# Kernel tuning notes

Hardware: AMD Instinct MI355X
Metric: run time of the kernel (lower is better)

Reference implementation:

```python
import jax, jax.numpy as jnp
import numpy as np

# dims: N nodes, E edges, C channel multiplicity, NS species, RB radial basis, H radial mlp hidden
N, E, C, NS, RB, H = 4000, 128000, 128, 5, 8, 64
AVG_N = 32.0  # avg_n_neighbors


def setup_inputs() -> dict:
    key = jax.random.key(0)
    ks = jax.random.split(key, 17)
    return {
        "x_scalars": jax.random.normal(ks[0], (N, C), jnp.float32),
        "x_vectors": jax.random.normal(ks[1], (N, C, 3), jnp.float32),
        "edge_vectors": jax.random.normal(ks[2], (E, 3), jnp.float32) * 2.0,
        "radial_basis": jax.random.normal(ks[3], (E, RB), jnp.float32),
        "W1_0": jax.random.normal(ks[4], (C, C), jnp.float32),
        "W1_1": jax.random.normal(ks[5], (C, C), jnp.float32),
        "rmlp_w0": jax.random.normal(ks[6], (RB, H), jnp.float32) * np.float32(np.sqrt(4.0 / RB)),
        "rmlp_w1": jax.random.normal(ks[7], (H, H), jnp.float32) * np.float32(np.sqrt(4.0 / H)),
        "rmlp_w2": jax.random.normal(ks[8], (H, H), jnp.float32) * np.float32(np.sqrt(4.0 / H)),
        "rmlp_w3": jax.random.normal(ks[9], (H, 4 * C), jnp.float32) * np.float32(np.sqrt(1.0 / H)),
        "W2_0": jax.random.normal(ks[10], (2 * C, 2 * C), jnp.float32),
        "W2_1": jax.random.normal(ks[11], (2 * C, C), jnp.float32),
        "Wsk0": jax.random.normal(ks[12], (NS, C, 2 * C), jnp.float32),
        "Wsk1": jax.random.normal(ks[13], (NS, C, C), jnp.float32),
        "species": jax.random.randint(ks[14], (N,), 0, NS),
        "senders": jax.random.randint(ks[15], (E,), 0, N),
        "receivers": jax.random.randint(ks[16], (E,), 0, N),
    }


def reference(x_scalars, x_vectors, edge_vectors, radial_basis,
              W1_0, W1_1, rmlp_w0, rmlp_w1, rmlp_w2, rmlp_w3,
              W2_0, W2_1, Wsk0, Wsk1, species, senders, receivers):
    n_nodes = x_scalars.shape[0]
    inv_c = 1.0 / jnp.sqrt(jnp.float32(C))
    # linear_1: per-irrep channel mixing (e3nn path-normalized Linear)
    y0 = (x_scalars @ W1_0) * inv_c                                  # [N,C] 0e
    y1 = jnp.einsum('nci,cd->ndi', x_vectors, W1_1) * inv_c          # [N,C,3] 1o
    # gather to edges
    m0 = y0[senders]                                                 # [E,C]
    m1 = y1[senders]                                                 # [E,C,3]
    # spherical harmonics lmax=1, component normalization: Y0=1, Y1=sqrt(3)*unit_vec
    r = jnp.linalg.norm(edge_vectors, axis=1, keepdims=True)
    u = edge_vectors / jnp.maximum(r, 1e-12)
    Y1 = jnp.sqrt(3.0) * u                                           # [E,3]
    # tensor product filtered to 0e,1o (explicit Clebsch-Gordan, component norm)
    t0a = m0                                                         # 0e x 0e -> 0e
    t0b = jnp.einsum('eci,ei->ec', m1, Y1) / jnp.sqrt(3.0)           # 1o x 1o -> 0e
    t1a = m0[:, :, None] * Y1[:, None, :]                            # 0e x 1o -> 1o
    t1b = m1                                                         # 1o x 0e -> 1o
    # radial MLP (silu, no bias), one scalar weight per tp irrep (4C total)
    h = jax.nn.silu(radial_basis @ rmlp_w0)
    h = jax.nn.silu(h @ rmlp_w1)
    h = jax.nn.silu(h @ rmlp_w2)
    w = h @ rmlp_w3                                                  # [E,4C]
    ws0, ws1 = w[:, :C], w[:, C:2 * C]
    wv0, wv1 = w[:, 2 * C:3 * C], w[:, 3 * C:]
    scal = jnp.concatenate([t0a * ws0, t0b * ws1], axis=1)           # [E,2C]
    vec = jnp.concatenate([t1a * wv0[:, :, None], t1b * wv1[:, :, None]], axis=1)  # [E,2C,3]
    # scatter-add to receivers, neighbor normalization
    inv_nb = 1.0 / jnp.sqrt(jnp.float32(AVG_N))
    agg_s = jax.ops.segment_sum(scal, receivers, num_segments=n_nodes) * inv_nb
    agg_v = jax.ops.segment_sum(vec, receivers, num_segments=n_nodes) * inv_nb
    # linear_2: tp irreps -> (2C)x0e + Cx1o  (C output scalars + C gates)
    inv_2c = 1.0 / jnp.sqrt(jnp.float32(2 * C))
    s = (agg_s @ W2_0) * inv_2c                                      # [N,2C]
    v = jnp.einsum('nci,cd->ndi', agg_v, W2_1) * inv_2c              # [N,C,3]
    # indexed (per-species) skip connection
    s = s + jnp.einsum('nc,ncd->nd', x_scalars, Wsk0[species]) * inv_c
    v = v + jnp.einsum('nci,ncd->ndi', x_vectors, Wsk1[species]) * inv_c
    # gate: silu on scalars, silu(gates) multiplies 1o features
    out_s = jax.nn.silu(s[:, :C])
    gates = jax.nn.silu(s[:, C:])
    out_v = v * gates[:, :, None]
    return jnp.concatenate([out_s, out_v.reshape(n_nodes, 3 * C)], axis=1)  # [N,4C]
```

## Files before the change

### kernel.cpp

```cpp
#include <hip/hip_runtime.h>
#include <math.h>

#define CC 128
#define HH 64
#define RBD 8
#define WDIM 512

typedef __attribute__((ext_vector_type(8))) short short8v;
typedef __attribute__((ext_vector_type(4))) float f32x4;

__device__ __forceinline__ float silu_f(float x) {
    return x / (1.0f + __expf(-x));
}

__device__ __forceinline__ unsigned short f2bf(float x) {
    unsigned int b = __float_as_uint(x);
    unsigned int r = (b + 0x7FFFu + ((b >> 16) & 1u)) >> 16;
    return (unsigned short)r;
}

__device__ __forceinline__ float bf2f(unsigned short u) {
    return __uint_as_float(((unsigned int)u) << 16);
}

__global__ void k_prep_hist(const float* __restrict__ w0, const float* __restrict__ w1,
                            const float* __restrict__ w2, const float* __restrict__ w3,
                            float* __restrict__ w0T, float* __restrict__ w1T,
                            float* __restrict__ w2T, float* __restrict__ w3T,
                            unsigned short* __restrict__ w3bs,
                            unsigned short* __restrict__ w0b,
                            unsigned short* __restrict__ w1b,
                            unsigned short* __restrict__ w2b,
                            const int* __restrict__ rcv, int* __restrict__ deg, int E_,
                            const int* __restrict__ species, int* __restrict__ scnt, int N) {
    int i = blockIdx.x * blockDim.x + threadIdx.x;
    if (i < E_) atomicAdd(&deg[rcv[i]], 1);
    if (i < N) atomicAdd(&scnt[species[i]], 1);
    if (i < 64 * 8) { int m = i / 8, k = i % 8; w0T[i] = w0[k * 64 + m]; }
    if (i < 64 * 64) { int m = i / 64, k = i % 64; w1T[i] = w1[k * 64 + m]; w2T[i] = w2[k * 64 + m]; }
    if (i < 512 * 64) { int j = i / 64, k = i % 64; w3T[i] = w3[k * 512 + j]; }
    if (i < 32768) {
        int t = i >> 10, ch = (i >> 9) & 1, lane = (i >> 3) & 63, j = i & 7;
        int k = ch * 32 + 8 * (lane >> 4) + j;
        int n = t * 16 + (lane & 15);
        w3bs[i] = f2bf(w3[k * 512 + n]);
    }
    if (i < 2048) {
        int t = i >> 9, lane = (i >> 3) & 63, j = i & 7;
        int k = 8 * (lane >> 4) + j;
        int col = t * 16 + (lane & 15);
        w0b[i] = (k < RBD) ? f2bf(w0[k * 64 + col]) : (unsigned short)0;
    }
    if (i < 4096) {
        int f = i >> 9, lane = (i >> 3) & 63, j = i & 7;
        int ks = f >> 2, t = f & 3;
        int k = ks * 32 + 8 * (lane >> 4) + j;
        int col = t * 16 + (lane & 15);
        w1b[i] = f2bf(w1[k * 64 + col]);
        w2b[i] = f2bf(w2[k * 64 + col]);
    }
}

__global__ __launch_bounds__(1024) void k_scan(const int* __restrict__ deg,
                                               int* __restrict__ off, int N,
                                               const int* __restrict__ scnt,
                                               int* __restrict__ soff, int NS) {
    __shared__ int s[1024];
    int t = threadIdx.x;
    int b = t * 4;
    int a0 = (b + 0 < N) ? deg[b + 0] : 0;
    int a1 = (b + 1 < N) ? deg[b + 1] : 0;
    int a2 = (b + 2 < N) ? deg[b + 2] : 0;
    int a3 = (b + 3 < N) ? deg[b + 3] : 0;
    int part = a0 + a1 + a2 + a3;
    s[t] = part;
    __syncthreads();
    for (int d = 1; d < 1024; d <<= 1) {
        int v = (t >= d) ? s[t - d] : 0;
        __syncthreads();
        s[t] += v;
        __syncthreads();
    }
    int excl = s[t] - part;
    if (b + 0 <= N) off[b + 0] = excl;
    if (b + 1 <= N) off[b + 1] = excl + a0;
    if (b + 2 <= N) off[b + 2] = excl + a0 + a1;
    if (b + 3 <= N) off[b + 3] = excl + a0 + a1 + a2;
    if (t == 0) {
        int acc = 0;
        for (int q = 0; q < NS; q++) { soff[q] = acc; acc += scnt[q]; }
        soff[NS] = acc;
    }
}

__global__ void k_scatter(const int* __restrict__ rcv, const int* __restrict__ off,
                          int* __restrict__ cur, int* __restrict__ elist, int E_,
                          const int* __restrict__ species, const int* __restrict__ soff,
                          int* __restrict__ scur, int* __restrict__ nlist, int N) {
    int e = blockIdx.x * blockDim.x + threadIdx.x;
    if (e < E_) {
        int r = rcv[e];
        int p = atomicAdd(&cur[r], 1);
        elist[off[r] + p] = e;
    }
    if (e < N) {
        int s = species[e];
        int p = atomicAdd(&scur[s], 1);
        nlist[soff[s] + p] = e;
    }
}

__global__ __launch_bounds__(256) void k_node_lin(
    const float* __restrict__ xs, const float* __restrict__ xv,
    const float* __restrict__ W10, const float* __restrict__ W11,
    float* __restrict__ y0, float* __restrict__ y1, int N) {
    const int tid = threadIdx.x;
    const int n0 = blockIdx.x * 2;
    const int NP = N * CC;
    const int d = tid & 127;
    const int nn = tid >> 7;
    const float inv_c = 0.08838834764831845f;

    __shared__ float xsl[2][128];
    __shared__ float xvl[2][384];
    xsl[tid >> 7][tid & 127] = xs[(size_t)n0 * 128 + tid];
    for (int i = tid; i < 768; i += 256) xvl[i / 384][i % 384] = xv[(size_t)n0 * 384 + i];
    __syncthreads();

    float a0 = 0.f, av0 = 0.f, av1 = 0.f, av2 = 0.f;
    #pragma unroll 4
    for (int c = 0; c < CC; c++) {
        float w10 = W10[c * CC + d];
        float w11 = W11[c * CC + d];
        float xsv = xsl[nn][c];
        a0 += xsv * w10;
        av0 += xvl[nn][c * 3 + 0] * w11;
        av1 += xvl[nn][c * 3 + 1] * w11;
        av2 += xvl[nn][c * 3 + 2] * w11;
    }
    y0[(size_t)(n0 + nn) * CC + d] = a0 * inv_c;
    y1[0 * NP + (size_t)(n0 + nn) * CC + d] = av0 * inv_c;
    y1[1 * NP + (size_t)(n0 + nn) * CC + d] = av1 * inv_c;
    y1[2 * NP + (size_t)(n0 + nn) * CC + d] = av2 * inv_c;
}

__device__ __forceinline__ void layer64(const float4* a, float4* b,
                                        const float* __restrict__ W) {
    #pragma unroll
    for (int m = 0; m < 16; m++) {
        float s0 = 0.f, s1 = 0.f, s2 = 0.f, s3 = 0.f;
        const float* w0p = W + (4 * m + 0) * 64;
        const float* w1p = W + (4 * m + 1) * 64;
        const float* w2p = W + (4 * m + 2) * 64;
        const float* w3p = W + (4 * m + 3) * 64;
        #pragma unroll
        for (int k = 0; k < 16; k++) {
            float4 av = a[k];
            s0 += av.x * w0p[4 * k + 0] + av.y * w0p[4 * k + 1] + av.z * w0p[4 * k + 2] + av.w * w0p[4 * k + 3];
            s1 += av.x * w1p[4 * k + 0] + av.y * w1p[4 * k + 1] + av.z * w1p[4 * k + 2] + av.w * w1p[4 * k + 3];
            s2 += av.x * w2p[4 * k + 0] + av.y * w2p[4 * k + 1] + av.z * w2p[4 * k + 2] + av.w * w2p[4 * k + 3];
            s3 += av.x * w3p[4 * k + 0] + av.y * w3p[4 * k + 1] + av.z * w3p[4 * k + 2] + av.w * w3p[4 * k + 3];
        }
        b[m] = make_float4(silu_f(s0), silu_f(s1), silu_f(s2), silu_f(s3));
    }
}

__device__ __forceinline__ void mlp_body(
    const float* __restrict__ rb, int e,
    const float* __restrict__ w0T, const float* __restrict__ w1T,
    const float* __restrict__ w2T, float4* a) {
    float rbv[RBD];
    #pragma unroll
    for (int k = 0; k < RBD; k++) rbv[k] = rb[(size_t)e * RBD + k];
    float4 b[16];
    #pragma unroll
    for (int m = 0; m < 16; m++) {
        float s0 = 0.f, s1 = 0.f, s2 = 0.f, s3 = 0.f;
        #pragma unroll
        for (int k = 0; k < RBD; k++) {
            float rv = rbv[k];
            s0 += rv * w0T[(4 * m + 0) * RBD + k];
            s1 += rv * w0T[(4 * m + 1) * RBD + k];
            s2 += rv * w0T[(4 * m + 2) * RBD + k];
            s3 += rv * w0T[(4 * m + 3) * RBD + k];
        }
        a[m] = make_float4(silu_f(s0), silu_f(s1), silu_f(s2), silu_f(s3));
    }
    layer64(a, b, w1T);
    layer64(b, a, w2T);
}

__global__ __launch_bounds__(256) void k_mlpw3(
    const float* __restrict__ rb, const int* __restrict__ elist,
    const int* __restrict__ snd, const float* __restrict__ evec,
    const unsigned short* __restrict__ w0b, const unsigned short* __restrict__ w1b,
    const unsigned short* __restrict__ w2b, const unsigned short* __restrict__ w3bs,
    unsigned int* __restrict__ Wq, float4* __restrict__ up, int* __restrict__ sp,
    int E_, int nblk_mlp,
    const float* __restrict__ xs, const float* __restrict__ xv,
    const float* __restrict__ W10, const float* __restrict__ W11,
    float* __restrict__ y0, float* __restrict__ y1, int NP) {
    __shared__ unsigned short hbuf[4][16][72];
    __shared__ float xsl[2][128];
    __shared__ float xvl[2][384];

    if (blockIdx.x >= nblk_mlp) {
        const int tid = threadIdx.x;
        const int n0 = (blockIdx.x - nblk_mlp) * 2;
        const int d = tid & 127;
        const int nn = tid >> 7;
        const float inv_c = 0.08838834764831845f;

        xsl[tid >> 7][tid & 127] = xs[(size_t)n0 * 128 + tid];
        for (int i = tid; i < 768; i += 256) xvl[i / 384][i % 384] = xv[(size_t)n0 * 384 + i];
        __syncthreads();

        float a0 = 0.f, av0 = 0.f, av1 = 0.f, av2 = 0.f;
        #pragma unroll 4
        for (int c = 0; c < CC; c++) {
            float w10 = W10[c * CC + d];
            float w11 = W11[c * CC + d];
            float xsv = xsl[nn][c];
            a0 += xsv * w10;
            av0 += xvl[nn][c * 3 + 0] * w11;
            av1 += xvl[nn][c * 3 + 1] * w11;
            av2 += xvl[nn][c * 3 + 2] * w11;
        }
        y0[(size_t)(n0 + nn) * CC + d] = a0 * inv_c;
        y1[0 * NP + (size_t)(n0 + nn) * CC + d] = av0 * inv_c;
        y1[1 * NP + (size_t)(n0 + nn) * CC + d] = av1 * inv_c;
        y1[2 * NP + (size_t)(n0 + nn) * CC + d] = av2 * inv_c;
        return;
    }

    const int lane = threadIdx.x & 63;
    const int wv = threadIdx.x >> 6;
    const int rbk = blockIdx.x * 4 + wv;
    const int col = lane & 15;
    const int grp = lane >> 4;

    if (threadIdx.x < 64) {
        int p = blockIdx.x * 64 + threadIdx.x;
        if (p < E_) {
            int e = elist[p];
            float e0 = evec[(size_t)e * 3 + 0];
            float e1 = evec[(size_t)e * 3 + 1];
            float e2 = evec[(size_t)e * 3 + 2];
            float rn = sqrtf(e0 * e0 + e1 * e1 + e2 * e2);
            float inv = 1.0f / fmaxf(rn, 1e-12f);
            up[p] = make_float4(e0 * inv, e1 * inv, e2 * inv, 0.f);
            sp[p] = snd[e];
        }
    }

    short8v a0 = (short8v){0, 0, 0, 0, 0, 0, 0, 0};
    if (grp == 0) {
        int e = elist[rbk * 16 + col];
        const float* rp = rb + (size_t)e * RBD;
        #pragma unroll
        for (int j = 0; j < RBD; j++) a0[j] = (short)f2bf(rp[j]);
    }
    f32x4 acc[4];
    {
        const unsigned short* bp = w0b + (size_t)lane * 8;
        #pragma unroll
        for (int t = 0; t < 4; t++) {
            short8v b = *(const short8v*)(bp + (size_t)t * 512);
            acc[t] = __builtin_amdgcn_mfma_f32_16x16x32_bf16(
                a0, b, (f32x4){0.f, 0.f, 0.f, 0.f}, 0, 0, 0);
        }
    }
    #pragma unroll
    for (int t = 0; t < 4; t++)
        #pragma unroll
        for (int r = 0; r < 4; r++)
            hbuf[wv][grp * 4 + r][t * 16 + col] = f2bf(silu_f(acc[t][r]));

    {
        short8v aA = *(const short8v*)&hbuf[wv][col][8 * grp];
        short8v aB = *(const short8v*)&hbuf[wv][col][32 + 8 * grp];
        const unsigned short* bp = w1b + (size_t)lane * 8;
        #pragma unroll
        for (int t = 0; t < 4; t++) {
            short8v b0 = *(const short8v*)(bp + (size_t)(0 + t) * 512);
            short8v b1 = *(const short8v*)(bp + (size_t)(4 + t) * 512);
            f32x4 c = __builtin_amdgcn_mfma_f32_16x16x32_bf16(
                aA, b0, (f32x4){0.f, 0.f, 0.f, 0.f}, 0, 0, 0);
            acc[t] = __builtin_amdgcn_mfma_f32_16x16x32_bf16(aB, b1, c, 0, 0, 0);
        }
    }
    #pragma unroll
    for (int t = 0; t < 4; t++)
        #pragma unroll
        for (int r = 0; r < 4; r++)
            hbuf[wv][grp * 4 + r][t * 16 + col] = f2bf(silu_f(acc[t][r]));

    {
        short8v aA = *(const short8v*)&hbuf[wv][col][8 * grp];
        short8v aB = *(const short8v*)&hbuf[wv][col][32 + 8 * grp];
        const unsigned short* bp = w2b + (size_t)lane * 8;
        #pragma unroll
        for (int t = 0; t < 4; t++) {
            short8v b0 = *(const short8v*)(bp + (size_t)(0 + t) * 512);
            short8v b1 = *(const short8v*)(bp + (size_t)(4 + t) * 512);
            f32x4 c = __builtin_amdgcn_mfma_f32_16x16x32_bf16(
                aA, b0, (f32x4){0.f, 0.f, 0.f, 0.f}, 0, 0, 0);
            acc[t] = __builtin_amdgcn_mfma_f32_16x16x32_bf16(aB, b1, c, 0, 0, 0);
        }
    }
    #pragma unroll
    for (int t = 0; t < 4; t++)
        #pragma unroll
        for (int r = 0; r < 4; r++)
            hbuf[wv][grp * 4 + r][t * 16 + col] = f2bf(silu_f(acc[t][r]));

    short8v A0 = *(const short8v*)&hbuf[wv][col][8 * grp];
    short8v A1 = *(const short8v*)&hbuf[wv][col][32 + 8 * grp];

    const unsigned short* bbase = w3bs + (size_t)lane * 8;
    const int rowq = grp * 4;
    const int jbase = rbk * 16 + rowq;

    #pragma unroll 1
    for (int pass = 0; pass < 2; pass++) {
        f32x4 wacc[16];
        #pragma unroll
        for (int q = 0; q < 16; q++) wacc[q] = (f32x4){0.f, 0.f, 0.f, 0.f};
        #pragma unroll
        for (int q = 0; q < 16; q++) {
            int t = (q < 8) ? (pass * 8 + q) : (16 + pass * 8 + (q - 8));
            short8v b0 = *(const short8v*)(bbase + (size_t)(t * 2 + 0) * 512);
            short8v b1 = *(const short8v*)(bbase + (size_t)(t * 2 + 1) * 512);
            wacc[q] = __builtin_amdgcn_mfma_f32_16x16x32_bf16(A0, b0, wacc[q], 0, 0, 0);
            wacc[q] = __builtin_amdgcn_mfma_f32_16x16x32_bf16(A1, b1, wacc[q], 0, 0, 0);
        }
        #pragma unroll
        for (int q = 0; q < 8; q++) {
            int t = pass * 8 + q;
            #pragma unroll
            for (int rr = 0; rr < 4; rr++) {
                unsigned lo = f2bf(wacc[q][rr]);
                unsigned hi = f2bf(wacc[q + 8][rr]);
                Wq[(size_t)(jbase + rr) * 256 + t * 16 + col] = lo | (hi << 16);
            }
        }
    }
}

__global__ __launch_bounds__(256, 4) void k_gather_em(
    const int* __restrict__ off, const float4* __restrict__ up,
    const int* __restrict__ sp, const unsigned int* __restrict__ Wq,
    const float* __restrict__ y0, const float* __restrict__ y1, int NP,
    float* __restrict__ agg_s, float* __restrict__ agg_v) {
    const int r = blockIdx.x;
    const int tid = threadIdx.x;
    const int half = tid >> 7;
    const int c = tid & 127;
    const int start = off[r];
    const int end = off[r + 1];

    float accs = 0.f, av0 = 0.f, av1 = 0.f, av2 = 0.f;
    const float SQ3 = 1.7320508075688772f;

    auto proc = [&](unsigned wq, float4 u, int s) {
        float wa = bf2f((unsigned short)(wq & 0xFFFFu));
        float wb = bf2f((unsigned short)(wq >> 16));
        if (half == 0) {
            float f = y0[(size_t)s * CC + c];
            accs += f * wa;
            float bb = f * wb * SQ3;
            av0 += bb * u.x; av1 += bb * u.y; av2 += bb * u.z;
        } else {
            float f0 = y1[0 * NP + s * CC + c];
            float f1 = y1[1 * NP + s * CC + c];
            float f2 = y1[2 * NP + s * CC + c];
            accs += (f0 * u.x + f1 * u.y + f2 * u.z) * wa;
            av0 += f0 * wb; av1 += f1 * wb; av2 += f2 * wb;
        }
    };

    int j = start;
    for (; j + 4 <= end; j += 4) {
        unsigned wq0 = Wq[(size_t)(j + 0) * 256 + tid];
        unsigned wq1 = Wq[(size_t)(j + 1) * 256 + tid];
        unsigned wq2 = Wq[(size_t)(j + 2) * 256 + tid];
        unsigned wq3 = Wq[(size_t)(j + 3) * 256 + tid];
        float4 u0 = up[j + 0], u1 = up[j + 1], u2 = up[j + 2], u3 = up[j + 3];
        int s0 = __builtin_amdgcn_readfirstlane(sp[j + 0]);
        int s1 = __builtin_amdgcn_readfirstlane(sp[j + 1]);
        int s2 = __builtin_amdgcn_readfirstlane(sp[j + 2]);
        int s3 = __builtin_amdgcn_readfirstlane(sp[j + 3]);
        proc(wq0, u0, s0);
        proc(wq1, u1, s1);
        proc(wq2, u2, s2);
        proc(wq3, u3, s3);
    }
    for (; j < end; j++) {
        unsigned wq = Wq[(size_t)j * 256 + tid];
        float4 u = up[j];
        int s = __builtin_amdgcn_readfirstlane(sp[j]);
        proc(wq, u, s);
    }

    agg_s[(size_t)r * 256 + tid] = accs;
    float* o = agg_v + ((size_t)r * 256 + tid) * 3;
    o[0] = av0; o[1] = av1; o[2] = av2;
}

__global__ __launch_bounds__(256) void k_mlp_wp(
    const float* __restrict__ rb, const int* __restrict__ elist,
    const float* __restrict__ w0T, const float* __restrict__ w1T,
    const float* __restrict__ w2T, const float* __restrict__ w3T,
    unsigned short* __restrict__ Wp, int E_) {
    int p = blockIdx.x * blockDim.x + threadIdx.x;
    if (p >= E_) return;
    int e = elist[p];
    const int c0 = blockIdx.y * 128;

    float4 a[16];
    mlp_body(rb, e, w0T, w1T, w2T, a);

    const size_t E4 = (size_t)E_ * 4;
    for (int c = c0; c < c0 + 128; c += 8) {
        float s[8];
        #pragma unroll
        for (int q = 0; q < 8; q++) {
            const float* rp = w3T + (size_t)(c + q) * 64;
            float t0 = 0.f, t1 = 0.f, t2 = 0.f, t3 = 0.f;
            #pragma unroll
            for (int k = 0; k < 16; k++) {
                float4 h = a[k];
                t0 += h.x * rp[4 * k + 0];
                t1 += h.y * rp[4 * k + 1];
                t2 += h.z * rp[4 * k + 2];
                t3 += h.w * rp[4 * k + 3];
            }
            s[q] = (t0 + t1) + (t2 + t3);
        }
        ushort4 pk0 = make_ushort4(f2bf(s[0]), f2bf(s[1]), f2bf(s[2]), f2bf(s[3]));
        ushort4 pk1 = make_ushort4(f2bf(s[4]), f2bf(s[5]), f2bf(s[6]), f2bf(s[7]));
        *(ushort4*)(Wp + (size_t)(c >> 2) * E4 + (size_t)p * 4) = pk0;
        *(ushort4*)(Wp + (size_t)((c >> 2) + 1) * E4 + (size_t)p * 4) = pk1;
    }
}

__global__ __launch_bounds__(512, 2) void k_gather_wg(
    const int* __restrict__ off, const int* __restrict__ elist,
    const int* __restrict__ snd, const float* __restrict__ evec,
    const unsigned short* __restrict__ Wp, int E_,
    const float* __restrict__ y0, const float* __restrict__ y1, int NP,
    float* __restrict__ agg_s, float* __restrict__ agg_v) {
    const int r = blockIdx.x;
    const int tid = threadIdx.x;
    const int part = tid >> 7;
    const int c = tid & 127;

    const int start = off[r];
    const int end = off[r + 1];

    const unsigned short* __restrict__ wstream =
        Wp + (size_t)(tid >> 2) * ((size_t)E_ * 4) + (tid & 3);

    float acc0 = 0.f, acc1 = 0.f, acc2 = 0.f;
    const float SQ3 = 1.7320508075688772f;

    #pragma unroll 2
    for (int j = start; j < end; j++) {
        int e = elist[j];
        e = __builtin_amdgcn_readfirstlane(e);
        int s = snd[e];
        s = __builtin_amdgcn_readfirstlane(s);

        float e0 = evec[(size_t)e * 3 + 0];
        float e1 = evec[(size_t)e * 3 + 1];
        float e2 = evec[(size_t)e * 3 + 2];
        float rn = sqrtf(e0 * e0 + e1 * e1 + e2 * e2);
        float inv = 1.0f / fmaxf(rn, 1e-12f);
        float ux = e0 * inv, uy = e1 * inv, uz = e2 * inv;

        float w = bf2f(wstream[(size_t)j * 4]);

        if (part == 0) {
            acc0 += y0[(size_t)s * CC + c] * w;
        } else if (part == 1) {
            float f = y1[0 * NP + s * CC + c] * ux
                    + y1[1 * NP + s * CC + c] * uy
                    + y1[2 * NP + s * CC + c] * uz;
            acc0 += f * w;
        } else if (part == 2) {
            float bb = y0[(size_t)s * CC + c] * w * SQ3;
            acc0 += bb * ux; acc1 += bb * uy; acc2 += bb * uz;
        } else {
            acc0 += y1[0 * NP + s * CC + c] * w;
            acc1 += y1[1 * NP + s * CC + c] * w;
            acc2 += y1[2 * NP + s * CC + c] * w;
        }
    }

    if (part == 0) {
        agg_s[(size_t)r * 256 + c] = acc0;
    } else if (part == 1) {
        agg_s[(size_t)r * 256 + 128 + c] = acc0;
    } else if (part == 2) {
        float* o = agg_v + ((size_t)r * 256 + c) * 3;
        o[0] = acc0; o[1] = acc1; o[2] = acc2;
    } else {
        float* o = agg_v + ((size_t)r * 256 + 128 + c) * 3;
        o[0] = acc0; o[1] = acc1; o[2] = acc2;
    }
}

__global__ void k_mlp(const float* __restrict__ rb,
                      const float* __restrict__ w0T, const float* __restrict__ w1T,
                      const float* __restrict__ w2T,
                      float* __restrict__ h2, int E_) {
    int e = blockIdx.x * blockDim.x + threadIdx.x;
    if (e >= E_) return;
    float4 a[16];
    mlp_body(rb, e, w0T, w1T, w2T, a);
    float4* out = (float4*)(h2 + (size_t)e * HH);
    #pragma unroll
    for (int q = 0; q < 16; q++) out[q] = a[q];
}

__global__ __launch_bounds__(512, 1) void k_gather_h2(
    const int* __restrict__ off, const int* __restrict__ elist,
    const int* __restrict__ snd, const float* __restrict__ evec,
    const float* __restrict__ h2, const float* __restrict__ w3T,
    const float* __restrict__ y0, const float* __restrict__ y1, int NP,
    float* __restrict__ agg_s, float* __restrict__ agg_v) {
    const int r = blockIdx.x;
    const int tid = threadIdx.x;
    const int part = tid >> 7;
    const int c = tid & 127;

    const float4* wp = (const float4*)(w3T + (size_t)tid * 64);
    const int start = off[r];
    const int end = off[r + 1];

    float acc0 = 0.f, acc1 = 0.f, acc2 = 0.f;
    const float SQ3 = 1.7320508075688772f;

    for (int j = start; j < end; j++) {
        int e = elist[j];
        e = __builtin_amdgcn_readfirstlane(e);
        int s = snd[e];
        s = __builtin_amdgcn_readfirstlane(s);

        float e0 = evec[(size_t)e * 3 + 0];
        float e1 = evec[(size_t)e * 3 + 1];
        float e2 = evec[(size_t)e * 3 + 2];
        float rn = sqrtf(e0 * e0 + e1 * e1 + e2 * e2);
        float inv = 1.0f / fmaxf(rn, 1e-12f);
        float ux = e0 * inv, uy = e1 * inv, uz = e2 * inv;

        const float4* __restrict__ hp = (const float4*)(h2 + ((size_t)e << 6));
        float ws0 = 0.f, ws1 = 0.f, ws2 = 0.f, ws3 = 0.f;
        #pragma unroll
        for (int k = 0; k < 16; k++) {
            float4 h = hp[k];
            float4 wv = wp[k];
            ws0 += h.x * wv.x; ws1 += h.y * wv.y; ws2 += h.z * wv.z; ws3 += h.w * wv.w;
        }
        float w = (ws0 + ws1) + (ws2 + ws3);

        if (part == 0) {
            acc0 += y0[(size_t)s * CC + c] * w;
        } else if (part == 1) {
            float f = y1[0 * NP + s * CC + c] * ux
                    + y1[1 * NP + s * CC + c] * uy
                    + y1[2 * NP + s * CC + c] * uz;
            acc0 += f * w;
        } else if (part == 2) {
            float bb = y0[(size_t)s * CC + c] * w * SQ3;
            acc0 += bb * ux; acc1 += bb * uy; acc2 += bb * uz;
        } else {
            acc0 += y1[0 * NP + s * CC + c] * w;
            acc1 += y1[1 * NP + s * CC + c] * w;
            acc2 += y1[2 * NP + s * CC + c] * w;
        }
    }

    if (part == 0) {
        agg_s[(size_t)r * 256 + c] = acc0;
    } else if (part == 1) {
        agg_s[(size_t)r * 256 + 128 + c] = acc0;
    } else if (part == 2) {
        float* o = agg_v + ((size_t)r * 256 + c) * 3;
        o[0] = acc0; o[1] = acc1; o[2] = acc2;
    } else {
        float* o = agg_v + ((size_t)r * 256 + 128 + c) * 3;
        o[0] = acc0; o[1] = acc1; o[2] = acc2;
    }
}

__global__ __launch_bounds__(256) void k_node_out(
    const float* __restrict__ agg_s, const float* __restrict__ agg_v,
    const float* __restrict__ xs, const float* __restrict__ xv,
    const float* __restrict__ W20, const float* __restrict__ W21,
    const float* __restrict__ Wsk0, const float* __restrict__ Wsk1,
    const int* __restrict__ nlist, const int* __restrict__ species,
    float* __restrict__ out, int N) {
    const int tid = threadIdx.x;
    const int b0 = blockIdx.x * 4;
    const int nid0 = nlist[min(b0 + 0, N - 1)];
    const int nid1 = nlist[min(b0 + 1, N - 1)];
    const int nid2 = nlist[min(b0 + 2, N - 1)];
    const int nid3 = nlist[min(b0 + 3, N - 1)];

    __shared__ float as_l[4 * 256];
    __shared__ float av_l[4 * 768];
    __shared__ float xs_l[4 * 128];
    __shared__ float xv_l[4 * 384];
    __shared__ float s_l[4 * 256];

    {
        as_l[0 * 256 + tid] = agg_s[(size_t)nid0 * 256 + tid];
        as_l[1 * 256 + tid] = agg_s[(size_t)nid1 * 256 + tid];
        as_l[2 * 256 + tid] = agg_s[(size_t)nid2 * 256 + tid];
        as_l[3 * 256 + tid] = agg_s[(size_t)nid3 * 256 + tid];
        for (int i = tid; i < 768; i += 256) {
            av_l[0 * 768 + i] = agg_v[(size_t)nid0 * 768 + i];
            av_l[1 * 768 + i] = agg_v[(size_t)nid1 * 768 + i];
            av_l[2 * 768 + i] = agg_v[(size_t)nid2 * 768 + i];
            av_l[3 * 768 + i] = agg_v[(size_t)nid3 * 768 + i];
        }
        if (tid < 128) {
            xs_l[0 * 128 + tid] = xs[(size_t)nid0 * 128 + tid];
            xs_l[1 * 128 + tid] = xs[(size_t)nid1 * 128 + tid];
            xs_l[2 * 128 + tid] = xs[(size_t)nid2 * 128 + tid];
            xs_l[3 * 128 + tid] = xs[(size_t)nid3 * 128 + tid];
        }
        for (int i = tid; i < 384; i += 256) {
            xv_l[0 * 384 + i] = xv[(size_t)nid0 * 384 + i];
            xv_l[1 * 384 + i] = xv[(size_t)nid1 * 384 + i];
            xv_l[2 * 384 + i] = xv[(size_t)nid2 * 384 + i];
            xv_l[3 * 384 + i] = xv[(size_t)nid3 * 384 + i];
        }
    }
    const int sp0 = species[nid0], sp1 = species[nid1];
    const int sp2 = species[nid2], sp3 = species[nid3];
    const bool uni = (sp0 == sp1) && (sp1 == sp2) && (sp2 == sp3);
    __syncthreads();

    const float k_mat = 0.17677669529663687f * 0.0625f;
    const float inv_c = 0.08838834764831845f;

    {
        const int d = tid;
        float am[4] = {0.f, 0.f, 0.f, 0.f};
        for (int cc = 0; cc < 256; cc++) {
            float w = W20[cc * 256 + d];
            #pragma unroll
            for (int n = 0; n < 4; n++) am[n] += as_l[n * 256 + cc] * w;
        }
        float ak[4] = {0.f, 0.f, 0.f, 0.f};
        if (uni) {
            for (int cc = 0; cc < 128; cc++) {
                float w = Wsk0[((size_t)sp0 * 128 + cc) * 256 + d];
                #pragma unroll
                for (int n = 0; n < 4; n++) ak[n] += xs_l[n * 128 + cc] * w;
            }
        } else {
            for (int cc = 0; cc < 128; cc++) {
                float w0v = Wsk0[((size_t)sp0 * 128 + cc) * 256 + d];
                float w1v = Wsk0[((size_t)sp1 * 128 + cc) * 256 + d];
                float w2v = Wsk0[((size_t)sp2 * 128 + cc) * 256 + d];
                float w3v = Wsk0[((size_t)sp3 * 128 + cc) * 256 + d];
                ak[0] += xs_l[0 * 128 + cc] * w0v;
                ak[1] += xs_l[1 * 128 + cc] * w1v;
                ak[2] += xs_l[2 * 128 + cc] * w2v;
                ak[3] += xs_l[3 * 128 + cc] * w3v;
            }
        }
        #pragma unroll
        for (int n = 0; n < 4; n++) s_l[n * 256 + d] = am[n] * k_mat + ak[n] * inv_c;
    }
    __syncthreads();

    if (tid < 128) {
        out[(size_t)nid0 * 512 + tid] = silu_f(s_l[0 * 256 + tid]);
        out[(size_t)nid1 * 512 + tid] = silu_f(s_l[1 * 256 + tid]);
        out[(size_t)nid2 * 512 + tid] = silu_f(s_l[2 * 256 + tid]);
        out[(size_t)nid3 * 512 + tid] = silu_f(s_l[3 * 256 + tid]);
    }

    {
        const int d = tid & 127;
        const int half = tid >> 7;
        const int nA = half ? nid2 : nid0;
        const int nB = half ? nid3 : nid1;
        const int sA = half ? sp2 : sp0;
        const int sB = half ? sp3 : sp1;
        const int la = half ? 2 : 0;
        const int lb = half ? 3 : 1;

        float am[2][3] = {};
        for (int cc = 0; cc < 256; cc++) {
            float w = W21[cc * 128 + d];
            #pragma unroll
            for (int i = 0; i < 3; i++) {
                am[0][i] += av_l[la * 768 + cc * 3 + i] * w;
                am[1][i] += av_l[lb * 768 + cc * 3 + i] * w;
            }
        }
        float ak[2][3] = {};
        if (uni) {
            for (int cc = 0; cc < 128; cc++) {
                float w = Wsk1[((size_t)sp0 * 128 + cc) * 128 + d];
                #pragma unroll
                for (int i = 0; i < 3; i++) {
                    ak[0][i] += xv_l[la * 384 + cc * 3 + i] * w;
                    ak[1][i] += xv_l[lb * 384 + cc * 3 + i] * w;
                }
            }
        } else {
            for (int cc = 0; cc < 128; cc++) {
                float wA = Wsk1[((size_t)sA * 128 + cc) * 128 + d];
                float wB = Wsk1[((size_t)sB * 128 + cc) * 128 + d];
                #pragma unroll
                for (int i = 0; i < 3; i++) {
                    ak[0][i] += xv_l[la * 384 + cc * 3 + i] * wA;
                    ak[1][i] += xv_l[lb * 384 + cc * 3 + i] * wB;
                }
            }
        }
        float gA = silu_f(s_l[la * 256 + 128 + d]);
        float gB = silu_f(s_l[lb * 256 + 128 + d]);
        float* oA = out + (size_t)nA * 512 + 128 + d * 3;
        float* oB = out + (size_t)nB * 512 + 128 + d * 3;
        #pragma unroll
        for (int i = 0; i < 3; i++) {
            oA[i] = (am[0][i] * k_mat + ak[0][i] * inv_c) * gA;
            oB[i] = (am[1][i] * k_mat + ak[1][i] * inv_c) * gB;
        }
    }
}

extern "C" void kernel_launch(void* const* d_in, const int* in_sizes, int n_in,
                              void* d_out, int out_size, void* d_ws, size_t ws_size,
                              hipStream_t stream) {
    const float* xs   = (const float*)d_in[0];
    const float* xv   = (const float*)d_in[1];
    const float* evec = (const float*)d_in[2];
    const float* rb   = (const float*)d_in[3];
    const float* W10  = (const float*)d_in[4];
    const float* W11  = (const float*)d_in[5];
    const float* w0   = (const float*)d_in[6];
    const float* w1   = (const float*)d_in[7];
    const float* w2   = (const float*)d_in[8];
    const float* w3   = (const float*)d_in[9];
    const float* W20  = (const float*)d_in[10];
    const float* W21  = (const float*)d_in[11];
    const float* Wsk0 = (const float*)d_in[12];
    const float* Wsk1 = (const float*)d_in[13];
    const int* species = (const int*)d_in[14];
    const int* snd = (const int*)d_in[15];
    const int* rcv = (const int*)d_in[16];

    const int N = in_sizes[0] / CC;
    const int E = in_sizes[2] / 3;
    const int NP = N * CC;
    int NS = in_sizes[12] / (CC * 2 * CC);
    if (NS < 1) NS = 1;
    if (NS > 63) NS = 63;

    float* ws   = (float*)d_ws;
    float* y0   = ws;
    float* y1   = y0 + (size_t)N * CC;
    float* aggs = y1 + (size_t)N * CC * 3;
    float* aggv = aggs + (size_t)N * 2 * CC;
    float* w0T  = aggv + (size_t)N * 2 * CC * 3;
    float* w1T  = w0T + 64 * 8;
    float* w2T  = w1T + 64 * 64;
    float* w3T  = w2T + 64 * 64;
    unsigned short* w3bs = (unsigned short*)(w3T + 512 * 64);
    unsigned short* w0b  = w3bs + 32768;
    unsigned short* w1b  = w0b + 2048;
    unsigned short* w2b  = w1b + 4096;
    int*   deg  = (int*)(w2b + 4096);
    int*   cur  = deg + 4096;
    int*   scnt = cur + 4096;
    int*   soff = scnt + 64;
    int*   scur = soff + 72;
    int*   off  = scur + 64;
    int*   elist = off + 4160;
    float4* up  = (float4*)(elist + E);
    int*   sp   = (int*)(up + E);
    int*   nlist = sp + E;
    void*  big  = (void*)(nlist + N);

    size_t base_bytes = (size_t)((char*)big - (char*)d_ws);
    size_t wq_bytes   = (size_t)E * 256 * sizeof(unsigned int);
    size_t need_A = base_bytes + wq_bytes;
    size_t need_B = base_bytes + (size_t)E * WDIM * sizeof(unsigned short);

    unsigned int*   Wq  = (unsigned int*)big;
    unsigned short* Wp  = (unsigned short*)big;

    hipMemsetAsync(deg, 0, (4096 + 4096 + 64 + 72 + 64) * sizeof(int), stream);
    hipLaunchKernelGGL(k_prep_hist, dim3((E + 255) / 256), dim3(256), 0, stream,
                       w0, w1, w2, w3, w0T, w1T, w2T, w3T, w3bs, w0b, w1b, w2b,
                       rcv, deg, E, species, scnt, N);
    hipLaunchKernelGGL(k_scan, dim3(1), dim3(1024), 0, stream,
                       deg, off, N, scnt, soff, NS);
    hipLaunchKernelGGL(k_scatter, dim3((E + 255) / 256), dim3(256), 0, stream,
                       rcv, off, cur, elist, E, species, soff, scur, nlist, N);

    if (ws_size >= need_A && (E % 64) == 0 && (N % 2) == 0) {
        const int nblk_mlp = E / 64;
        hipLaunchKernelGGL(k_mlpw3, dim3(nblk_mlp + N / 2), dim3(256), 0, stream,
                           rb, elist, snd, evec, w0b, w1b, w2b, w3bs, Wq, up, sp,
                           E, nblk_mlp, xs, xv, W10, W11, y0, y1, NP);
        hipLaunchKernelGGL(k_gather_em, dim3(N), dim3(256), 0, stream,
                           off, up, sp, Wq, y0, y1, NP, aggs, aggv);
    } else if (ws_size >= need_B) {
        hipLaunchKernelGGL(k_node_lin, dim3((N + 1) / 2), dim3(256), 0, stream,
                           xs, xv, W10, W11, y0, y1, N);
        hipLaunchKernelGGL(k_mlp_wp, dim3((E + 255) / 256, 4), dim3(256), 0, stream,
                           rb, elist, w0T, w1T, w2T, w3T, Wp, E);
        hipLaunchKernelGGL(k_gather_wg, dim3(N), dim3(512), 0, stream,
                           off, elist, snd, evec, Wp, E, y0, y1, NP, aggs, aggv);
    } else {
        hipLaunchKernelGGL(k_node_lin, dim3((N + 1) / 2), dim3(256), 0, stream,
                           xs, xv, W10, W11, y0, y1, N);
        hipLaunchKernelGGL(k_mlp, dim3((E + 255) / 256), dim3(256), 0, stream,
                           rb, w0T, w1T, w2T, (float*)big, E);
        hipLaunchKernelGGL(k_gather_h2, dim3(N), dim3(512), 0, stream,
                           off, elist, snd, evec, (const float*)big, w3T,
                           y0, y1, NP, aggs, aggv);
    }

    hipLaunchKernelGGL(k_node_out, dim3((N + 3) / 4), dim3(256), 0, stream,
                       aggs, aggv, xs, xv, W20, W21, Wsk0, Wsk1, nlist, species,
                       (float*)d_out, N);
}
```

Baseline: 244.9 us.

## Fuse edge gather aggregation with node output linear, skip and gate kernel

Merges the per-receiver gather/aggregate kernel with the node output stage. Each block now handles four species-sorted nodes, keeps the aggregated features in shared memory and applies W2, the per-species skip and the gate directly, so agg_s/agg_v are never written to or read back from global memory. It also switches the bf16 packing in the MLP kernel to the hardware v_cvt_pk_bf16_f32 instruction. The cost is lower parallelism in the gather phase (one block per four nodes instead of one per node, with the four nodes processed serially) and a drop from the occupancy hint of 4.

```diff
diff --git a/kernel.cpp b/kernel.cpp
--- a/kernel.cpp
+++ b/kernel.cpp
@@ -21,6 +21,12 @@
 
 __device__ __forceinline__ float bf2f(unsigned short u) {
     return __uint_as_float(((unsigned int)u) << 16);
+}
+
+__device__ __forceinline__ unsigned cvt_pk_bf16(float lo, float hi) {
+    unsigned r;
+    asm("v_cvt_pk_bf16_f32 %0, %1, %2" : "=v"(r) : "v"(lo), "v"(hi));
+    return r;
 }
 
 __global__ void k_prep_hist(const float* __restrict__ w0, const float* __restrict__ w1,
@@ -339,72 +345,198 @@
             int t = pass * 8 + q;
             #pragma unroll
             for (int rr = 0; rr < 4; rr++) {
-                unsigned lo = f2bf(wacc[q][rr]);
-                unsigned hi = f2bf(wacc[q + 8][rr]);
-                Wq[(size_t)(jbase + rr) * 256 + t * 16 + col] = lo | (hi << 16);
-            }
-        }
-    }
-}
-
-__global__ __launch_bounds__(256, 4) void k_gather_em(
+                Wq[(size_t)(jbase + rr) * 256 + t * 16 + col] =
+                    cvt_pk_bf16(wacc[q][rr], wacc[q + 8][rr]);
+            }
+        }
+    }
+}
+
+__global__ __launch_bounds__(256) void k_gno(
     const int* __restrict__ off, const float4* __restrict__ up,
-    const int* __restrict__ sp, const unsigned int* __restrict__ Wq,
+    const int* __restrict__ sp_, const unsigned int* __restrict__ Wq,
     const float* __restrict__ y0, const float* __restrict__ y1, int NP,
-    float* __restrict__ agg_s, float* __restrict__ agg_v) {
-    const int r = blockIdx.x;
+    const float* __restrict__ xs, const float* __restrict__ xv,
+    const float* __restrict__ W20, const float* __restrict__ W21,
+    const float* __restrict__ Wsk0, const float* __restrict__ Wsk1,
+    const int* __restrict__ nlist, const int* __restrict__ species,
+    float* __restrict__ out, int N) {
     const int tid = threadIdx.x;
+    const int b0 = blockIdx.x * 4;
+    int nids[4];
+    #pragma unroll
+    for (int n = 0; n < 4; n++) nids[n] = nlist[min(b0 + n, N - 1)];
+
+    __shared__ float as_l[4 * 256];
+    __shared__ float av_l[4 * 768];
+    __shared__ float xs_l[4 * 128];
+    __shared__ float xv_l[4 * 384];
+    __shared__ float s_l[4 * 256];
+
+    if (tid < 128) {
+        #pragma unroll
+        for (int n = 0; n < 4; n++)
+            xs_l[n * 128 + tid] = xs[(size_t)nids[n] * 128 + tid];
+    }
+    for (int i = tid; i < 384; i += 256) {
+        #pragma unroll
+        for (int n = 0; n < 4; n++)
+            xv_l[n * 384 + i] = xv[(size_t)nids[n] * 384 + i];
+    }
+
     const int half = tid >> 7;
     const int c = tid & 127;
-    const int start = off[r];
-    const int end = off[r + 1];
-
-    float accs = 0.f, av0 = 0.f, av1 = 0.f, av2 = 0.f;
     const float SQ3 = 1.7320508075688772f;
 
-    auto proc = [&](unsigned wq, float4 u, int s) {
-        float wa = bf2f((unsigned short)(wq & 0xFFFFu));
-        float wb = bf2f((unsigned short)(wq >> 16));
-        if (half == 0) {
-            float f = y0[(size_t)s * CC + c];
-            accs += f * wa;
-            float bb = f * wb * SQ3;
-            av0 += bb * u.x; av1 += bb * u.y; av2 += bb * u.z;
+    #pragma unroll
+    for (int n = 0; n < 4; n++) {
+        const int nid = nids[n];
+        const int start = off[nid];
+        const int end = off[nid + 1];
+        float accs = 0.f, av0 = 0.f, av1 = 0.f, av2 = 0.f;
+
+        auto proc = [&](unsigned wq, float4 u, int s) {
+            float wa = bf2f((unsigned short)(wq & 0xFFFFu));
+            float wb = bf2f((unsigned short)(wq >> 16));
+            if (half == 0) {
+                float f = y0[(size_t)s * CC + c];
+                accs += f * wa;
+                float bb = f * wb * SQ3;
+                av0 += bb * u.x; av1 += bb * u.y; av2 += bb * u.z;
+            } else {
+                float f0 = y1[0 * NP + s * CC + c];
+                float f1 = y1[1 * NP + s * CC + c];
+                float f2 = y1[2 * NP + s * CC + c];
+                accs += (f0 * u.x + f1 * u.y + f2 * u.z) * wa;
+                av0 += f0 * wb; av1 += f1 * wb; av2 += f2 * wb;
+            }
+        };
+
+        int j = start;
+        for (; j + 4 <= end; j += 4) {
+            unsigned wq0 = Wq[(size_t)(j + 0) * 256 + tid];
+            unsigned wq1 = Wq[(size_t)(j + 1) * 256 + tid];
+            unsigned wq2 = Wq[(size_t)(j + 2) * 256 + tid];
+            unsigned wq3 = Wq[(size_t)(j + 3) * 256 + tid];
+            float4 u0 = up[j + 0], u1 = up[j + 1], u2 = up[j + 2], u3 = up[j + 3];
+            int s0 = __builtin_amdgcn_readfirstlane(sp_[j + 0]);
+            int s1 = __builtin_amdgcn_readfirstlane(sp_[j + 1]);
+            int s2 = __builtin_amdgcn_readfirstlane(sp_[j + 2]);
+            int s3 = __builtin_amdgcn_readfirstlane(sp_[j + 3]);
+            proc(wq0, u0, s0);
+            proc(wq1, u1, s1);
+            proc(wq2, u2, s2);
+            proc(wq3, u3, s3);
+        }
+        for (; j < end; j++) {
+            unsigned wq = Wq[(size_t)j * 256 + tid];
+            float4 u = up[j];
+            int s = __builtin_amdgcn_readfirstlane(sp_[j]);
+            proc(wq, u, s);
+        }
+
+        as_l[n * 256 + tid] = accs;
+        av_l[n * 768 + tid * 3 + 0] = av0;
+        av_l[n * 768 + tid * 3 + 1] = av1;
+        av_l[n * 768 + tid * 3 + 2] = av2;
+    }
+
+    const int sp0 = species[nids[0]], sp1 = species[nids[1]];
+    const int sp2 = species[nids[2]], sp3 = species[nids[3]];
+    const bool uni = (sp0 == sp1) && (sp1 == sp2) && (sp2 == sp3);
+    __syncthreads();
+
+    const float k_mat = 0.17677669529663687f * 0.0625f;
+    const float inv_c = 0.08838834764831845f;
+
+    {
+        const int d = tid;
+        float am[4] = {0.f, 0.f, 0.f, 0.f};
+        for (int cc = 0; cc < 256; cc++) {
+            float w = W20[cc * 256 + d];
+            #pragma unroll
+            for (int n = 0; n < 4; n++) am[n] += as_l[n * 256 + cc] * w;
+        }
+        float ak[4] = {0.f, 0.f, 0.f, 0.f};
+        if (uni) {
+            for (int cc = 0; cc < 128; cc++) {
+                float w = Wsk0[((size_t)sp0 * 128 + cc) * 256 + d];
+                #pragma unroll
+                for (int n = 0; n < 4; n++) ak[n] += xs_l[n * 128 + cc] * w;
+            }
         } else {
-            float f0 = y1[0 * NP + s * CC + c];
-            float f1 = y1[1 * NP + s * CC + c];
-            float f2 = y1[2 * NP + s * CC + c];
-            accs += (f0 * u.x + f1 * u.y + f2 * u.z) * wa;
-            av0 += f0 * wb; av1 += f1 * wb; av2 += f2 * wb;
-        }
-    };
-
-    int j = start;
-    for (; j + 4 <= end; j += 4) {
-        unsigned wq0 = Wq[(size_t)(j + 0) * 256 + tid];
-        unsigned wq1 = Wq[(size_t)(j + 1) * 256 + tid];
-        unsigned wq2 = Wq[(size_t)(j + 2) * 256 + tid];
-        unsigned wq3 = Wq[(size_t)(j + 3) * 256 + tid];
-        float4 u0 = up[j + 0], u1 = up[j + 1], u2 = up[j + 2], u3 = up[j + 3];
-        int s0 = __builtin_amdgcn_readfirstlane(sp[j + 0]);
-        int s1 = __builtin_amdgcn_readfirstlane(sp[j + 1]);
-        int s2 = __builtin_amdgcn_readfirstlane(sp[j + 2]);
-        int s3 = __builtin_amdgcn_readfirstlane(sp[j + 3]);
-        proc(wq0, u0, s0);
-        proc(wq1, u1, s1);
-        proc(wq2, u2, s2);
-        proc(wq3, u3, s3);
-    }
-    for (; j < end; j++) {
-        unsigned wq = Wq[(size_t)j * 256 + tid];
-        float4 u = up[j];
-        int s = __builtin_amdgcn_readfirstlane(sp[j]);
-        proc(wq, u, s);
-    }
-
-    agg_s[(size_t)r * 256 + tid] = accs;
-    float* o = agg_v + ((size_t)r * 256 + tid) * 3;
-    o[0] = av0; o[1] = av1; o[2] = av2;
+            for (int cc = 0; cc < 128; cc++) {
+                float w0v = Wsk0[((size_t)sp0 * 128 + cc) * 256 + d];
+                float w1v = Wsk0[((size_t)sp1 * 128 + cc) * 256 + d];
+                float w2v = Wsk0[((size_t)sp2 * 128 + cc) * 256 + d];
+                float w3v = Wsk0[((size_t)sp3 * 128 + cc) * 256 + d];
+                ak[0] += xs_l[0 * 128 + cc] * w0v;
+                ak[1] += xs_l[1 * 128 + cc] * w1v;
+                ak[2] += xs_l[2 * 128 + cc] * w2v;
+                ak[3] += xs_l[3 * 128 + cc] * w3v;
+            }
+        }
+        #pragma unroll
+        for (int n = 0; n < 4; n++) s_l[n * 256 + d] = am[n] * k_mat + ak[n] * inv_c;
+    }
+    __syncthreads();
+
+    if (tid < 128) {
+        out[(size_t)nids[0] * 512 + tid] = silu_f(s_l[0 * 256 + tid]);
+        out[(size_t)nids[1] * 512 + tid] = silu_f(s_l[1 * 256 + tid]);
+        out[(size_t)nids[2] * 512 + tid] = silu_f(s_l[2 * 256 + tid]);
+        out[(size_t)nids[3] * 512 + tid] = silu_f(s_l[3 * 256 + tid]);
+    }
+
+    {
+        const int d = tid & 127;
+        const int nA = half ? nids[2] : nids[0];
+        const int nB = half ? nids[3] : nids[1];
+        const int sA = half ? sp2 : sp0;
+        const int sB = half ? sp3 : sp1;
+        const int la = half ? 2 : 0;
+        const int lb = half ? 3 : 1;
+
+        float am[2][3] = {};
+        for (int cc = 0; cc < 256; cc++) {
+            float w = W21[cc * 128 + d];
+            #pragma unroll
+            for (int i = 0; i < 3; i++) {
+                am[0][i] += av_l[la * 768 + cc * 3 + i] * w;
+                am[1][i] += av_l[lb * 768 + cc * 3 + i] * w;
+            }
+        }
+        float ak[2][3] = {};
+        if (uni) {
+            for (int cc = 0; cc < 128; cc++) {
+                float w = Wsk1[((size_t)sp0 * 128 + cc) * 128 + d];
+                #pragma unroll
+                for (int i = 0; i < 3; i++) {
+                    ak[0][i] += xv_l[la * 384 + cc * 3 + i] * w;
+                    ak[1][i] += xv_l[lb * 384 + cc * 3 + i] * w;
+                }
+            }
+        } else {
+            for (int cc = 0; cc < 128; cc++) {
+                float wA = Wsk1[((size_t)sA * 128 + cc) * 128 + d];
+                float wB = Wsk1[((size_t)sB * 128 + cc) * 128 + d];
+                #pragma unroll
+                for (int i = 0; i < 3; i++) {
+                    ak[0][i] += xv_l[la * 384 + cc * 3 + i] * wA;
+                    ak[1][i] += xv_l[lb * 384 + cc * 3 + i] * wB;
+                }
+            }
+        }
+        float gA = silu_f(s_l[la * 256 + 128 + d]);
+        float gB = silu_f(s_l[lb * 256 + 128 + d]);
+        float* oA = out + (size_t)nA * 512 + 128 + d * 3;
+        float* oB = out + (size_t)nB * 512 + 128 + d * 3;
+        #pragma unroll
+        for (int i = 0; i < 3; i++) {
+            oA[i] = (am[0][i] * k_mat + ak[0][i] * inv_c) * gA;
+            oB[i] = (am[1][i] * k_mat + ak[1][i] * inv_c) * gB;
+        }
+    }
 }
 
 __global__ __launch_bounds__(256) void k_mlp_wp(
@@ -812,8 +944,10 @@
         hipLaunchKernelGGL(k_mlpw3, dim3(nblk_mlp + N / 2), dim3(256), 0, stream,
                            rb, elist, snd, evec, w0b, w1b, w2b, w3bs, Wq, up, sp,
                            E, nblk_mlp, xs, xv, W10, W11, y0, y1, NP);
-        hipLaunchKernelGGL(k_gather_em, dim3(N), dim3(256), 0, stream,
-                           off, up, sp, Wq, y0, y1, NP, aggs, aggv);
+        hipLaunchKernelGGL(k_gno, dim3((N + 3) / 4), dim3(256), 0, stream,
+                           off, up, sp, Wq, y0, y1, NP, xs, xv,
+                           W20, W21, Wsk0, Wsk1, nlist, species,
+                           (float*)d_out, N);
     } else if (ws_size >= need_B) {
         hipLaunchKernelGGL(k_node_lin, dim3((N + 1) / 2), dim3(256), 0, stream,
                            xs, xv, W10, W11, y0, y1, N);
@@ -821,6 +955,9 @@
                            rb, elist, w0T, w1T, w2T, w3T, Wp, E);
         hipLaunchKernelGGL(k_gather_wg, dim3(N), dim3(512), 0, stream,
                            off, elist, snd, evec, Wp, E, y0, y1, NP, aggs, aggv);
+        hipLaunchKernelGGL(k_node_out, dim3((N + 3) / 4), dim3(256), 0, stream,
+                           aggs, aggv, xs, xv, W20, W21, Wsk0, Wsk1, nlist, species,
+                           (float*)d_out, N);
     } else {
         hipLaunchKernelGGL(k_node_lin, dim3((N + 1) / 2), dim3(256), 0, stream,
                            xs, xv, W10, W11, y0, y1, N);
@@ -829,9 +966,8 @@
         hipLaunchKernelGGL(k_gather_h2, dim3(N), dim3(512), 0, stream,
                            off, elist, snd, evec, (const float*)big, w3T,
                            y0, y1, NP, aggs, aggv);
-    }
-
-    hipLaunchKernelGGL(k_node_out, dim3((N + 3) / 4), dim3(256), 0, stream,
-                       aggs, aggv, xs, xv, W20, W21, Wsk0, Wsk1, nlist, species,
-                       (float*)d_out, N);
-}
+        hipLaunchKernelGGL(k_node_out, dim3((N + 3) / 4), dim3(256), 0, stream,
+                           aggs, aggv, xs, xv, W20, W21, Wsk0, Wsk1, nlist, species,
+                           (float*)d_out, N);
+    }
+}
```

New measurement: 253.5 us. 3.5% more time.
